# Kernel tuning notes

Measured on AMD Instinct MI355X. Metric: run time of the kernel, lower is better.

The kernel has to match this reference:

```python
import jax, jax.numpy as jnp
import numpy as np

USER_COUNT = 200000
ITEM_COUNT = 100000
N_NODES = USER_COUNT + ITEM_COUNT
EMB = 64
NNZ = 9600000
N_LAYERS = 3
BATCH = 4096
VAL_SCALE = 0.03125  # ~1/avg_degree, mimics symmetric degree normalization of norm_adj


def setup_inputs() -> dict:
    key = jax.random.key(0)
    k1, k2, k3, k4, k5, k6, k7 = jax.random.split(key, 7)
    user_emb = jax.random.normal(k1, (USER_COUNT, EMB), dtype=jnp.float32)
    item_emb = jax.random.normal(k2, (ITEM_COUNT, EMB), dtype=jnp.float32)
    adj_row = jnp.sort(jax.random.randint(k3, (NNZ,), 0, N_NODES, dtype=jnp.int64))
    adj_col = jax.random.randint(k4, (NNZ,), 0, N_NODES, dtype=jnp.int64)
    adj_val = jax.random.uniform(k5, (NNZ,), dtype=jnp.float32) * VAL_SCALE
    users = jax.random.randint(k6, (BATCH,), 0, USER_COUNT, dtype=jnp.int64)
    items = jax.random.randint(k7, (BATCH,), 0, ITEM_COUNT, dtype=jnp.int64)
    return {"user_emb": user_emb, "item_emb": item_emb, "adj_row": adj_row,
            "adj_col": adj_col, "adj_val": adj_val, "users": users, "items": items}


def _spmm(row, col, val, x):
    # sparse [N,N] @ dense [N,E] via gather + segment-sum
    return jax.ops.segment_sum(val[:, None] * x[col], row, num_segments=N_NODES)


def reference(user_emb, item_emb, adj_row, adj_col, adj_val, users, items):
    ego = jnp.concatenate([user_emb, item_emb], axis=0)  # [N, E]
    acc = ego  # running sum across layer outputs (== stack+mean fused)
    h = ego
    for _ in range(N_LAYERS):
        h = _spmm(adj_row, adj_col, adj_val, h)
        acc = acc + h
    all_emb = acc / jnp.float32(N_LAYERS + 1)
    u_all = all_emb[:USER_COUNT]
    i_all = all_emb[USER_COUNT:]
    return (u_all[users], i_all[items])
```

## Files before the change

kernel.cpp:

```cpp
#include <hip/hip_runtime.h>

#define USER_COUNT 200000
#define ITEM_COUNT 100000
#define N_NODES    300000
#define EMB        64
#define BATCH      4096

typedef unsigned int   u32;
typedef unsigned char  u8;
typedef float float2v  __attribute__((ext_vector_type(2)));
typedef float float8v  __attribute__((ext_vector_type(8)));
typedef u32   u32x2    __attribute__((ext_vector_type(2)));

static __device__ __forceinline__ u32 pk4_fp8(float a, float b, float c, float d) {
    u32 w = 0;
    w = (u32)__builtin_amdgcn_cvt_pk_fp8_f32(a, b, (int)w, false);
    w = (u32)__builtin_amdgcn_cvt_pk_fp8_f32(c, d, (int)w, true);
    return w;
}
static __device__ __forceinline__ void unpk4_fp8(u32 w, float* o) {
    float2v lo = __builtin_amdgcn_cvt_pk_f32_fp8((int)w, false);
    float2v hi = __builtin_amdgcn_cvt_pk_f32_fp8((int)w, true);
    o[0] = lo.x; o[1] = lo.y; o[2] = hi.x; o[3] = hi.y;
}

__global__ void prep_kernel(const int* __restrict__ row,
                            int* __restrict__ ptr,
                            const float* __restrict__ ue,
                            const float* __restrict__ ie,
                            u32* __restrict__ out8, int nnz) {
    size_t t = (size_t)blockIdx.x * blockDim.x + threadIdx.x;

    if (t < (size_t)nnz) {
        int i = (int)t;
        int r  = row[i];
        int rp = (i == 0) ? -1 : row[i - 1];
        for (int rr = rp + 1; rr <= r; ++rr) ptr[rr] = i;
        if (i == nnz - 1) {
            for (int rr = r + 1; rr <= N_NODES; ++rr) ptr[rr] = nnz;
        }
    }

    const size_t total = (size_t)N_NODES * EMB / 4;
    if (t < total) {
        size_t base = t * 4;
        const size_t ub = (size_t)USER_COUNT * EMB;
        const float* src = (base < ub) ? (ue + base) : (ie + (base - ub));
        float4 v = *(const float4*)src;
        out8[t] = pk4_fp8(v.x, v.y, v.z, v.w);
    }
}

__global__ void mark_needed(const int* __restrict__ users,
                            const int* __restrict__ items,
                            const int* __restrict__ col,
                            const int* __restrict__ ptr,
                            u32* __restrict__ flag) {
    int slot = (int)((blockIdx.x * blockDim.x + threadIdx.x) >> 6);
    if (slot >= 2 * BATCH) return;
    int lane = threadIdx.x & 63;
    int row = (slot < BATCH) ? users[slot] : (items[slot - BATCH] + USER_COUNT);
    if (lane == 0) flag[row] = 1;
    int p0 = ptr[row];
    int p1 = ptr[row + 1];
    for (int j = p0 + lane; j < p1; j += 64) flag[col[j]] = 1;
}

#define SLOT_REDUCE(ACC)                                              \
    _Pragma("unroll")                                                 \
    for (int q = 0; q < 8; ++q) {                                     \
        ACC[q] += __shfl_xor(ACC[q], 8, 64);                          \
        ACC[q] += __shfl_xor(ACC[q], 16, 64);                         \
        ACC[q] += __shfl_xor(ACC[q], 32, 64);                         \
    }

static __device__ __forceinline__ float8v row_accum(
        const u8* __restrict__ x, const int* __restrict__ col,
        const float* __restrict__ val, int p0, int p1, int e, int d) {
    float8v a0 = {0,0,0,0,0,0,0,0};
    float8v a1 = {0,0,0,0,0,0,0,0};
    float8v a2 = {0,0,0,0,0,0,0,0};
    float8v a3 = {0,0,0,0,0,0,0,0};

    int base = p0;
    for (; base + 32 <= p1; base += 32) {
        int j0 = base + e, j1 = j0 + 8, j2 = j0 + 16, j3 = j0 + 24;
        int   c0 = __builtin_nontemporal_load(col + j0);
        int   c1 = __builtin_nontemporal_load(col + j1);
        int   c2 = __builtin_nontemporal_load(col + j2);
        int   c3 = __builtin_nontemporal_load(col + j3);
        float v0 = __builtin_nontemporal_load(val + j0);
        float v1 = __builtin_nontemporal_load(val + j1);
        float v2 = __builtin_nontemporal_load(val + j2);
        float v3 = __builtin_nontemporal_load(val + j3);
        u32x2 h0 = *(const u32x2*)(x + (size_t)c0 * EMB + d);
        u32x2 h1 = *(const u32x2*)(x + (size_t)c1 * EMB + d);
        u32x2 h2 = *(const u32x2*)(x + (size_t)c2 * EMB + d);
        u32x2 h3 = *(const u32x2*)(x + (size_t)c3 * EMB + d);
        float xf[8];
        unpk4_fp8(h0.x, xf); unpk4_fp8(h0.y, xf + 4);
        #pragma unroll
        for (int q = 0; q < 8; ++q) a0[q] += v0 * xf[q];
        unpk4_fp8(h1.x, xf); unpk4_fp8(h1.y, xf + 4);
        #pragma unroll
        for (int q = 0; q < 8; ++q) a1[q] += v1 * xf[q];
        unpk4_fp8(h2.x, xf); unpk4_fp8(h2.y, xf + 4);
        #pragma unroll
        for (int q = 0; q < 8; ++q) a2[q] += v2 * xf[q];
        unpk4_fp8(h3.x, xf); unpk4_fp8(h3.y, xf + 4);
        #pragma unroll
        for (int q = 0; q < 8; ++q) a3[q] += v3 * xf[q];
    }

    if (base < p1) {
        int p1m1 = p1 - 1;
        int jj0 = base + e, jj1 = jj0 + 8, jj2 = jj0 + 16, jj3 = jj0 + 24;
        int jc0 = (jj0 < p1) ? jj0 : p1m1;
        int jc1 = (jj1 < p1) ? jj1 : p1m1;
        int jc2 = (jj2 < p1) ? jj2 : p1m1;
        int jc3 = (jj3 < p1) ? jj3 : p1m1;
        int   c0 = __builtin_nontemporal_load(col + jc0);
        int   c1 = __builtin_nontemporal_load(col + jc1);
        int   c2 = __builtin_nontemporal_load(col + jc2);
        int   c3 = __builtin_nontemporal_load(col + jc3);
        float v0 = __builtin_nontemporal_load(val + jc0);
        float v1 = __builtin_nontemporal_load(val + jc1);
        float v2 = __builtin_nontemporal_load(val + jc2);
        float v3 = __builtin_nontemporal_load(val + jc3);
        v0 = (jj0 < p1) ? v0 : 0.0f;
        v1 = (jj1 < p1) ? v1 : 0.0f;
        v2 = (jj2 < p1) ? v2 : 0.0f;
        v3 = (jj3 < p1) ? v3 : 0.0f;
        u32x2 h0 = *(const u32x2*)(x + (size_t)c0 * EMB + d);
        u32x2 h1 = *(const u32x2*)(x + (size_t)c1 * EMB + d);
        u32x2 h2 = *(const u32x2*)(x + (size_t)c2 * EMB + d);
        u32x2 h3 = *(const u32x2*)(x + (size_t)c3 * EMB + d);
        float xf[8];
        unpk4_fp8(h0.x, xf); unpk4_fp8(h0.y, xf + 4);
        #pragma unroll
        for (int q = 0; q < 8; ++q) a0[q] += v0 * xf[q];
        unpk4_fp8(h1.x, xf); unpk4_fp8(h1.y, xf + 4);
        #pragma unroll
        for (int q = 0; q < 8; ++q) a1[q] += v1 * xf[q];
        unpk4_fp8(h2.x, xf); unpk4_fp8(h2.y, xf + 4);
        #pragma unroll
        for (int q = 0; q < 8; ++q) a2[q] += v2 * xf[q];
        unpk4_fp8(h3.x, xf); unpk4_fp8(h3.y, xf + 4);
        #pragma unroll
        for (int q = 0; q < 8; ++q) a3[q] += v3 * xf[q];
    }

    #pragma unroll
    for (int q = 0; q < 8; ++q) a0[q] += (a1[q] + a2[q]) + a3[q];
    return a0;
}

template <bool USE_FLAG>
__global__ __launch_bounds__(256) void spmm_fp8(
        const u8* __restrict__ x, const int* __restrict__ col,
        const float* __restrict__ val, const int* __restrict__ ptr,
        const u32* __restrict__ flag, u8* __restrict__ y) {
    int wave = (int)((blockIdx.x * blockDim.x + threadIdx.x) >> 6);
    int lane = threadIdx.x & 63;
    if (wave >= N_NODES) return;
    if (USE_FLAG && flag[wave] == 0) return;
    int e = lane >> 3;
    int d = (lane & 7) << 3;

    int p0 = ptr[wave];
    int p1 = ptr[wave + 1];

    float8v a = row_accum(x, col, val, p0, p1, e, d);
    SLOT_REDUCE(a);

    if (e == 0) {
        u32x2 o;
        o.x = pk4_fp8(a[0], a[1], a[2], a[3]);
        o.y = pk4_fp8(a[4], a[5], a[6], a[7]);
        __builtin_nontemporal_store(o, (u32x2*)(y + (size_t)wave * EMB + d));
    }
}

__global__ __launch_bounds__(256) void finalize(
        const u8* __restrict__ h1, const u8* __restrict__ h2,
        const float* __restrict__ ue, const float* __restrict__ ie,
        const int* __restrict__ col, const float* __restrict__ val,
        const int* __restrict__ ptr, const int* __restrict__ users,
        const int* __restrict__ items, float* __restrict__ out) {
    int slot = (int)((blockIdx.x * blockDim.x + threadIdx.x) >> 6);
    if (slot >= 2 * BATCH) return;
    int lane = threadIdx.x & 63;
    int e = lane >> 3;
    int d = (lane & 7) << 3;

    int row = (slot < BATCH) ? users[slot] : (items[slot - BATCH] + USER_COUNT);
    int p0 = ptr[row];
    int p1 = ptr[row + 1];

    float8v a = row_accum(h2, col, val, p0, p1, e, d);
    SLOT_REDUCE(a);

    if (e == 0) {
        const float* eg = ((row < USER_COUNT) ? (ue + (size_t)row * EMB)
                                              : (ie + (size_t)(row - USER_COUNT) * EMB)) + d;
        u32x2 w1 = *(const u32x2*)(h1 + (size_t)row * EMB + d);
        u32x2 w2 = *(const u32x2*)(h2 + (size_t)row * EMB + d);
        float f1[8], f2[8];
        unpk4_fp8(w1.x, f1); unpk4_fp8(w1.y, f1 + 4);
        unpk4_fp8(w2.x, f2); unpk4_fp8(w2.y, f2 + 4);
        float4 o0, o1;
        o0.x = 0.25f * (eg[0] + f1[0] + f2[0] + a[0]);
        o0.y = 0.25f * (eg[1] + f1[1] + f2[1] + a[1]);
        o0.z = 0.25f * (eg[2] + f1[2] + f2[2] + a[2]);
        o0.w = 0.25f * (eg[3] + f1[3] + f2[3] + a[3]);
        o1.x = 0.25f * (eg[4] + f1[4] + f2[4] + a[4]);
        o1.y = 0.25f * (eg[5] + f1[5] + f2[5] + a[5]);
        o1.z = 0.25f * (eg[6] + f1[6] + f2[6] + a[6]);
        o1.w = 0.25f * (eg[7] + f1[7] + f2[7] + a[7]);
        float* o = out + (size_t)slot * EMB + d;
        *(float4*)o       = o0;
        *(float4*)(o + 4) = o1;
    }
}

extern "C" void kernel_launch(void* const* d_in, const int* in_sizes, int n_in,
                              void* d_out, int out_size, void* d_ws, size_t ws_size,
                              hipStream_t stream) {
    const float* user_emb = (const float*)d_in[0];
    const float* item_emb = (const float*)d_in[1];
    const int*   adj_row  = (const int*)d_in[2];
    const int*   adj_col  = (const int*)d_in[3];
    const float* adj_val  = (const float*)d_in[4];
    const int*   users    = (const int*)d_in[5];
    const int*   items    = (const int*)d_in[6];
    float*       out      = (float*)d_out;
    const int    nnz      = in_sizes[2];

    char* ws = (char*)d_ws;
    const size_t hbytes = (size_t)N_NODES * EMB;
    u8*  ego8 = (u8*)(ws);
    u8*  h1   = (u8*)(ws + hbytes);
    u8*  h2   = (u8*)(ws + 2 * hbytes);
    int* ptr  = (int*)(ws + 3 * hbytes);
    u32* flag = (u32*)(ws + 3 * hbytes + (size_t)(N_NODES + 64) * sizeof(int));

    (void)hipMemsetAsync(flag, 0, (size_t)N_NODES * sizeof(u32), stream);

    prep_kernel<<<(nnz + 255) / 256, 256, 0, stream>>>(
        adj_row, ptr, user_emb, item_emb, (u32*)ego8, nnz);

    mark_needed<<<(2 * BATCH + 3) / 4, 256, 0, stream>>>(
        users, items, adj_col, ptr, flag);

    const int spmm_blocks = (N_NODES + 3) / 4;
    const int sel_blocks  = (2 * BATCH + 3) / 4;

    spmm_fp8<false><<<spmm_blocks, 256, 0, stream>>>(
        ego8, adj_col, adj_val, ptr, nullptr, h1);

    spmm_fp8<true><<<spmm_blocks, 256, 0, stream>>>(
        h1, adj_col, adj_val, ptr, flag, h2);

    finalize<<<sel_blocks, 256, 0, stream>>>(
        h1, h2, user_emb, item_emb, adj_col, adj_val, ptr, users, items, out);
}
```

Measured before the change: 341.8 us.

## Partition SpMM columns into four slices to localize gathers in cache

Adds a bucketing pass that reorders each row's nonzeros by column slice (four slices of 75k nodes), then runs SpMM per slice so concurrent blocks gather from a smaller region of the fp8 embedding table, writing fp8 partials that a separate kernel sums. The aim is to cut cache misses on random gathers. In exchange it adds a full pass over col/val each call, extra partial writes and reads, an extra fp8 rounding step per partial, and it falls back to the old path if workspace is too small.

Measured after the change: 1.025 ms. 200% more time.

```diff
diff --git a/kernel.cpp b/kernel.cpp
--- a/kernel.cpp
+++ b/kernel.cpp
@@ -5,8 +5,11 @@
 #define N_NODES    300000
 #define EMB        64
 #define BATCH      4096
+#define NSLICE     4
+#define SLICE_W    75000
 
 typedef unsigned int   u32;
+typedef unsigned long long u64;
 typedef unsigned char  u8;
 typedef float float2v  __attribute__((ext_vector_type(2)));
 typedef float float8v  __attribute__((ext_vector_type(8)));
@@ -22,6 +25,11 @@
     float2v lo = __builtin_amdgcn_cvt_pk_f32_fp8((int)w, false);
     float2v hi = __builtin_amdgcn_cvt_pk_f32_fp8((int)w, true);
     o[0] = lo.x; o[1] = lo.y; o[2] = hi.x; o[3] = hi.y;
+}
+
+static __device__ __forceinline__ int slice_of(int c) {
+    return (c >= 2 * SLICE_W) ? ((c >= 3 * SLICE_W) ? 3 : 2)
+                              : ((c >= SLICE_W) ? 1 : 0);
 }
 
 __global__ void prep_kernel(const int* __restrict__ row,
@@ -48,6 +56,59 @@
         const float* src = (base < ub) ? (ue + base) : (ie + (base - ub));
         float4 v = *(const float4*)src;
         out8[t] = pk4_fp8(v.x, v.y, v.z, v.w);
+    }
+}
+
+__global__ __launch_bounds__(256) void bucket_kernel(
+        const int* __restrict__ col, const float* __restrict__ val,
+        const int* __restrict__ ptr, int* __restrict__ offA,
+        int* __restrict__ colB, float* __restrict__ valB) {
+    int rowi = (int)((blockIdx.x * blockDim.x + threadIdx.x) >> 6);
+    if (rowi >= N_NODES) return;
+    int lane = (int)(threadIdx.x & 63);
+    int p0 = ptr[rowi], p1 = ptr[rowi + 1];
+
+    int c0 = 0, c1 = 0, c2 = 0, c3 = 0;
+    for (int j0 = p0; j0 < p1; j0 += 64) {
+        int j = j0 + lane;
+        bool act = j < p1;
+        int c = col[act ? j : (p1 - 1)];
+        int s = slice_of(c);
+        c0 += (int)__popcll(__ballot(act && s == 0));
+        c1 += (int)__popcll(__ballot(act && s == 1));
+        c2 += (int)__popcll(__ballot(act && s == 2));
+        c3 += (int)__popcll(__ballot(act && s == 3));
+    }
+    int off0 = p0, off1 = off0 + c0, off2 = off1 + c1, off3 = off2 + c2;
+    if (lane == 0) {
+        offA[0 * N_NODES + rowi] = off0;
+        offA[1 * N_NODES + rowi] = off1;
+        offA[2 * N_NODES + rowi] = off2;
+        offA[3 * N_NODES + rowi] = off3;
+    }
+
+    int w0 = 0, w1 = 0, w2 = 0, w3 = 0;
+    u64 below = ((u64)1 << lane) - 1;
+    for (int j0 = p0; j0 < p1; j0 += 64) {
+        int j = j0 + lane;
+        bool act = j < p1;
+        int jc = act ? j : (p1 - 1);
+        int c = col[jc];
+        float v = val[jc];
+        int s = slice_of(c);
+        u64 b0 = __ballot(act && s == 0);
+        u64 b1 = __ballot(act && s == 1);
+        u64 b2 = __ballot(act && s == 2);
+        u64 b3 = __ballot(act && s == 3);
+        u64 bs = (s == 0) ? b0 : (s == 1) ? b1 : (s == 2) ? b2 : b3;
+        int wb = (s == 0) ? w0 : (s == 1) ? w1 : (s == 2) ? w2 : w3;
+        int ob = (s == 0) ? off0 : (s == 1) ? off1 : (s == 2) ? off2 : off3;
+        int dest = ob + wb + (int)__popcll(bs & below);
+        if (act) { colB[dest] = c; valB[dest] = v; }
+        w0 += (int)__popcll(b0);
+        w1 += (int)__popcll(b1);
+        w2 += (int)__popcll(b2);
+        w3 += (int)__popcll(b3);
     }
 }
 
@@ -156,6 +217,57 @@
 }
 
 template <bool USE_FLAG>
+__global__ __launch_bounds__(256) void spmm_slice(
+        const u8* __restrict__ x, const int* __restrict__ colB,
+        const float* __restrict__ valB, const int* __restrict__ offA,
+        const int* __restrict__ ptr, const u32* __restrict__ flag,
+        u8* __restrict__ partial) {
+    int b = blockIdx.x;
+    int s = b & 3;
+    int row = ((b >> 2) << 2) + (int)(threadIdx.x >> 6);
+    if (row >= N_NODES) return;
+    if (USE_FLAG && flag[row] == 0) return;
+    int lane = threadIdx.x & 63;
+    int e = lane >> 3;
+    int d = (lane & 7) << 3;
+
+    int p0 = offA[s * N_NODES + row];
+    int p1 = (s < 3) ? offA[(s + 1) * N_NODES + row] : ptr[row + 1];
+
+    float8v a = row_accum(x, colB, valB, p0, p1, e, d);
+    SLOT_REDUCE(a);
+
+    if (e == 0) {
+        u32x2 o;
+        o.x = pk4_fp8(a[0], a[1], a[2], a[3]);
+        o.y = pk4_fp8(a[4], a[5], a[6], a[7]);
+        __builtin_nontemporal_store(
+            o, (u32x2*)(partial + ((size_t)s * N_NODES + row) * EMB + d));
+    }
+}
+
+__global__ void reduce_partials(const u8* __restrict__ partial,
+                                u8* __restrict__ y) {
+    size_t t = (size_t)blockIdx.x * blockDim.x + threadIdx.x;
+    const size_t total = (size_t)N_NODES * (EMB / 8);
+    if (t >= total) return;
+    size_t byteoff = t * 8;
+    float acc[8] = {0,0,0,0,0,0,0,0};
+    #pragma unroll
+    for (int s = 0; s < NSLICE; ++s) {
+        u32x2 wv = *(const u32x2*)(partial + (size_t)s * N_NODES * EMB + byteoff);
+        float f[8];
+        unpk4_fp8(wv.x, f); unpk4_fp8(wv.y, f + 4);
+        #pragma unroll
+        for (int q = 0; q < 8; ++q) acc[q] += f[q];
+    }
+    u32x2 o;
+    o.x = pk4_fp8(acc[0], acc[1], acc[2], acc[3]);
+    o.y = pk4_fp8(acc[4], acc[5], acc[6], acc[7]);
+    __builtin_nontemporal_store(o, (u32x2*)(y + byteoff));
+}
+
+template <bool USE_FLAG>
 __global__ __launch_bounds__(256) void spmm_fp8(
         const u8* __restrict__ x, const int* __restrict__ col,
         const float* __restrict__ val, const int* __restrict__ ptr,
@@ -166,13 +278,10 @@
     if (USE_FLAG && flag[wave] == 0) return;
     int e = lane >> 3;
     int d = (lane & 7) << 3;
-
     int p0 = ptr[wave];
     int p1 = ptr[wave + 1];
-
     float8v a = row_accum(x, col, val, p0, p1, e, d);
     SLOT_REDUCE(a);
-
     if (e == 0) {
         u32x2 o;
         o.x = pk4_fp8(a[0], a[1], a[2], a[3]);
@@ -237,12 +346,19 @@
     const int    nnz      = in_sizes[2];
 
     char* ws = (char*)d_ws;
-    const size_t hbytes = (size_t)N_NODES * EMB;
+    const size_t hbytes  = (size_t)N_NODES * EMB;
+    const size_t ibytes  = (size_t)(N_NODES + 64) * sizeof(int);
     u8*  ego8 = (u8*)(ws);
     u8*  h1   = (u8*)(ws + hbytes);
     u8*  h2   = (u8*)(ws + 2 * hbytes);
     int* ptr  = (int*)(ws + 3 * hbytes);
-    u32* flag = (u32*)(ws + 3 * hbytes + (size_t)(N_NODES + 64) * sizeof(int));
+    u32* flag = (u32*)(ws + 3 * hbytes + ibytes);
+    int*   offA    = (int*)(ws + 3 * hbytes + 2 * ibytes);
+    int*   colB    = (int*)((char*)offA + (size_t)NSLICE * N_NODES * sizeof(int));
+    float* valB    = (float*)((char*)colB + (size_t)nnz * sizeof(int));
+    u8*    partial = (u8*)((char*)valB + (size_t)nnz * sizeof(float));
+    size_t need = ((char*)partial + (size_t)NSLICE * hbytes) - ws;
+    bool sliced = need <= ws_size;
 
     (void)hipMemsetAsync(flag, 0, (size_t)N_NODES * sizeof(u32), stream);
 
@@ -255,11 +371,26 @@
     const int spmm_blocks = (N_NODES + 3) / 4;
     const int sel_blocks  = (2 * BATCH + 3) / 4;
 
-    spmm_fp8<false><<<spmm_blocks, 256, 0, stream>>>(
-        ego8, adj_col, adj_val, ptr, nullptr, h1);
-
-    spmm_fp8<true><<<spmm_blocks, 256, 0, stream>>>(
-        h1, adj_col, adj_val, ptr, flag, h2);
+    if (sliced) {
+        bucket_kernel<<<spmm_blocks, 256, 0, stream>>>(
+            adj_col, adj_val, ptr, offA, colB, valB);
+
+        const int slice_blocks = NSLICE * ((N_NODES + 3) / 4);
+        const int red_blocks   = (int)(((size_t)N_NODES * (EMB / 8) + 255) / 256);
+
+        spmm_slice<false><<<slice_blocks, 256, 0, stream>>>(
+            ego8, colB, valB, offA, ptr, nullptr, partial);
+        reduce_partials<<<red_blocks, 256, 0, stream>>>(partial, h1);
+
+        spmm_slice<true><<<slice_blocks, 256, 0, stream>>>(
+            h1, colB, valB, offA, ptr, flag, partial);
+        reduce_partials<<<red_blocks, 256, 0, stream>>>(partial, h2);
+    } else {
+        spmm_fp8<false><<<spmm_blocks, 256, 0, stream>>>(
+            ego8, adj_col, adj_val, ptr, nullptr, h1);
+        spmm_fp8<true><<<spmm_blocks, 256, 0, stream>>>(
+            h1, adj_col, adj_val, ptr, flag, h2);
+    }
 
     finalize<<<sel_blocks, 256, 0, stream>>>(
         h1, h2, user_emb, item_emb, adj_col, adj_val, ptr, users, items, out);
```
